# Performance work log

Hardware: AMD Instinct MI355X
Metric: run time of the kernel (lower is better)

The kernel has to match this reference:

```python
import jax, jax.numpy as jnp
import numpy as np

NUM_QUBITS = 10
LAYERS = 8
DIM = 2 ** NUM_QUBITS  # 1024


def _build_entangling(nq: int) -> jnp.ndarray:
    """Static chain-of-CNOTs entangling block, D x D complex64."""
    I = np.eye(2)
    cnot = np.array([[1, 0, 0, 0], [0, 1, 0, 0], [0, 0, 0, 1], [0, 0, 1, 0]], dtype=np.float64)
    M = np.eye(2 ** nq)
    layers = []
    for i in range(nq - 1):
        mats = [I] * nq
        mats[i] = cnot
        del mats[i + 1]
        out = np.eye(1)
        for m in mats:
            out = np.kron(out, m)
        layers.append(out)
    for L in reversed(layers):
        M = L @ M
    return jnp.asarray(M, dtype=jnp.complex64)


ENTANGLING = _build_entangling(NUM_QUBITS)


def _r3(angles):
    # angles: [B, 3] (omega, theta, phi) -> [B, 2, 2] complex64 R3 gate
    omega, theta, phi = angles[:, 0], angles[:, 1], angles[:, 2]
    c = jnp.cos(theta / 2).astype(jnp.complex64)
    s = jnp.sin(theta / 2).astype(jnp.complex64)
    m11 = jnp.exp(-0.5j * (phi + omega)) * c
    m12 = -jnp.exp(0.5j * (phi - omega)) * s
    m21 = jnp.exp(-0.5j * (phi - omega)) * s
    m22 = jnp.exp(0.5j * (phi + omega)) * c
    return jnp.stack([jnp.stack([m11, m12], -1), jnp.stack([m21, m22], -1)], -2)


def _batched_kron(a, b):
    # a: [B, m, n], b: [B, p, q] -> [B, m*p, n*q]
    B = a.shape[0]
    return jnp.einsum('bij,bkl->bikjl', a, b).reshape(B, a.shape[1] * b.shape[1], a.shape[2] * b.shape[2])


def _rotation_block(angles):
    # angles: [copies, num_qubits, 3] -> [copies, D, D] complex64
    out = _r3(angles[:, 0])
    for q in range(1, NUM_QUBITS):
        out = _batched_kron(out, _r3(angles[:, q]))
    return out


def setup_inputs() -> dict:
    key = jax.random.key(0)
    k1, k2 = jax.random.split(key)
    inp = jax.random.normal(k1, (128, DIM), dtype=jnp.float32)
    params = jax.random.normal(k2, (32, LAYERS, NUM_QUBITS, 3), dtype=jnp.float32)
    return {"input": inp, "params": params}


def reference(input, params):
    copies = params.shape[0]
    batch = input.shape[0] // copies
    M0 = jnp.broadcast_to(jnp.eye(DIM, dtype=jnp.complex64), (copies, DIM, DIM))
    xs = jnp.moveaxis(params, 1, 0)  # [layers, copies, nq, 3]

    def step(M, p):
        M = jnp.matmul(_rotation_block(p), M)         # rotation layer
        M = jnp.einsum('ij,bjk->bik', ENTANGLING, M)  # entangling layer
        return M, None

    M, _ = jax.lax.scan(step, M0, xs)
    M = jnp.repeat(M, batch, axis=0)                  # [copies*batch, D, D]
    x = input.astype(jnp.complex64)
    return jnp.einsum('bij,bj->bi', M, x)
```

## Files before the change

kernel.cpp:

```cpp
#include <hip/hip_runtime.h>


#define DIM 1024
#define NQ 10
#define NLAYERS 8
#define NGATES (NLAYERS * NQ)

__device__ __forceinline__ unsigned short f2bf(float f) {
    unsigned int u = __float_as_uint(f);
    unsigned int r = u + 0x7FFFu + ((u >> 16) & 1u);
    return (unsigned short)(r >> 16);
}

__global__ __launch_bounds__(512) void
UnitaryR3Ansatz_18846316495450_kernel(const float* __restrict__ inp,
                                      const float* __restrict__ params,
                                      void* __restrict__ outp,
                                      int out_size)
{
    __shared__ float gates[NGATES][8];
    __shared__ float2 bufA[DIM];
    __shared__ float2 bufB[DIM];

    const int b = blockIdx.x;
    const int c = b >> 2;
    const int t = threadIdx.x;

    if (t < NGATES) {
        const float* p = params + c * (NLAYERS * NQ * 3) + t * 3;
        const float omega = p[0], theta = p[1], phi = p[2];
        float sh, ch;  sincosf(0.5f * theta, &sh, &ch);
        float sa, ca;  sincosf(0.5f * (phi + omega), &sa, &ca);
        float sb, cb;  sincosf(0.5f * (phi - omega), &sb, &cb);
        gates[t][0] = ca * ch;  gates[t][1] = -sa * ch;
        gates[t][2] = -cb * sh; gates[t][3] = -sb * sh;
        gates[t][4] = cb * sh;  gates[t][5] = -sb * sh;
        gates[t][6] = ca * ch;  gates[t][7] = sa * ch;
    }

    const float* x = inp + b * DIM;
    bufA[t]       = make_float2(x[t], 0.0f);
    bufA[t + 512] = make_float2(x[t + 512], 0.0f);

    float2* cur = bufA;
    float2* nxt = bufB;

    for (int l = 0; l < NLAYERS; ++l) {
        for (int q = 0; q < NQ; ++q) {
            __syncthreads();
            const int k = 9 - q;
            const int s = 1 << k;
            const int i0 = ((t >> k) << (k + 1)) | (t & (s - 1));
            const int i1 = i0 | s;
            const float* g = gates[l * NQ + q];
            const float2 a0 = cur[i0];
            const float2 a1 = cur[i1];
            float2 n0, n1;
            n0.x = g[0] * a0.x - g[1] * a0.y + g[2] * a1.x - g[3] * a1.y;
            n0.y = g[0] * a0.y + g[1] * a0.x + g[2] * a1.y + g[3] * a1.x;
            n1.x = g[4] * a0.x - g[5] * a0.y + g[6] * a1.x - g[7] * a1.y;
            n1.y = g[4] * a0.y + g[5] * a0.x + g[6] * a1.y + g[7] * a1.x;
            cur[i0] = n0;
            cur[i1] = n1;
        }
        __syncthreads();
        {
            const int x0 = t, x1 = t + 512;
            nxt[x0 ^ (x0 >> 1)] = cur[x0];
            nxt[x1 ^ (x1 >> 1)] = cur[x1];
        }
        float2* tmp = cur; cur = nxt; nxt = tmp;
    }

    __syncthreads();

    if (out_size >= 2 * DIM * 128) {
        ushort2* o2 = (ushort2*)outp + (size_t)b * DIM;
        for (int j = t; j < DIM; j += 512) {
            ushort2 v; v.x = f2bf(cur[j].x); v.y = f2bf(cur[j].y);
            o2[j] = v;
        }
    } else {
        float* of = (float*)outp + (size_t)b * DIM;
        for (int j = t; j < DIM; j += 512) {
            of[j] = cur[j].x;
        }
    }
}

extern "C" void kernel_launch(void* const* d_in, const int* in_sizes, int n_in,
                              void* d_out, int out_size, void* d_ws, size_t ws_size,
                              hipStream_t stream) {
    const float* inp    = (const float*)d_in[0];
    const float* params = (const float*)d_in[1];
    (void)in_sizes; (void)n_in; (void)d_ws; (void)ws_size;
    UnitaryR3Ansatz_18846316495450_kernel<<<128, 512, 0, stream>>>(inp, params, d_out, out_size);
}
```

Before: 72.12 us.

## Keep state vector in registers of one wavefront, using shuffles for gates

Each block becomes a single 64-lane wavefront that holds 16 amplitudes per lane in registers. Gates on low qubits are applied in-register, gates on high qubits use xor shuffles, and the Gray-code entangling permutation uses shuffles plus register swaps. This removes the 80 block-wide barriers and the shared-memory round-trips per sample. The cost is only 128 wavefronts in total, which leaves the GPU lightly occupied, plus heavy register pressure and many shuffle instructions.

```diff
diff --git a/kernel.cpp b/kernel.cpp
--- a/kernel.cpp
+++ b/kernel.cpp
@@ -4,7 +4,7 @@
 #define DIM 1024
 #define NQ 10
 #define NLAYERS 8
-#define NGATES (NLAYERS * NQ)
+#define NGATES 80
 
 __device__ __forceinline__ unsigned short f2bf(float f) {
     unsigned int u = __float_as_uint(f);
@@ -12,78 +12,135 @@
     return (unsigned short)(r >> 16);
 }
 
-__global__ __launch_bounds__(512) void
+__device__ __forceinline__ float2 cmadd2(float2 c0, float2 x0, float2 c1, float2 x1) {
+    float re = c0.x * x0.x - c0.y * x0.y + c1.x * x1.x - c1.y * x1.y;
+    float im = c0.x * x0.y + c0.y * x0.x + c1.x * x1.y + c1.y * x1.x;
+    return make_float2(re, im);
+}
+
+template <int K>
+__device__ __forceinline__ void local_gate(float2 (&a)[16], float2 m11, float2 m12,
+                                           float2 m21, float2 m22) {
+#pragma unroll
+    for (int p = 0; p < 8; ++p) {
+        const int i0 = ((p >> K) << (K + 1)) | (p & ((1 << K) - 1));
+        const int i1 = i0 | (1 << K);
+        const float2 a0 = a[i0];
+        const float2 a1 = a[i1];
+        a[i0] = cmadd2(m11, a0, m12, a1);
+        a[i1] = cmadd2(m21, a0, m22, a1);
+    }
+}
+
+template <int M>
+__device__ __forceinline__ void cross_gate(float2 (&a)[16], int lane, float2 m11,
+                                           float2 m12, float2 m21, float2 m22) {
+    const bool hi = (lane >> M) & 1;
+    const float2 cs = hi ? m22 : m11;
+    const float2 co = hi ? m21 : m12;
+#pragma unroll
+    for (int r = 0; r < 16; ++r) {
+        float2 o;
+        o.x = __shfl_xor(a[r].x, 1 << M, 64);
+        o.y = __shfl_xor(a[r].y, 1 << M, 64);
+        a[r] = cmadd2(cs, a[r], co, o);
+    }
+}
+
+__device__ __forceinline__ void gray_permute(float2 (&a)[16], int lane) {
+    int S = lane;
+    S ^= S >> 1; S ^= S >> 2; S ^= S >> 4;
+    S &= 63;
+    float2 tmp[16];
+#pragma unroll
+    for (int r = 0; r < 16; ++r) {
+        tmp[r].x = __shfl(a[r].x, S, 64);
+        tmp[r].y = __shfl(a[r].y, S, 64);
+    }
+#pragma unroll
+    for (int t = 0; t < 16; ++t) a[t ^ (t >> 1)] = tmp[t];
+    const bool s0 = S & 1;
+#pragma unroll
+    for (int s = 0; s < 8; ++s) {
+        const float2 lo = a[s], hi2 = a[s + 8];
+        a[s]     = s0 ? hi2 : lo;
+        a[s + 8] = s0 ? lo : hi2;
+    }
+}
+
+__global__ __launch_bounds__(64) void
 UnitaryR3Ansatz_18846316495450_kernel(const float* __restrict__ inp,
                                       const float* __restrict__ params,
                                       void* __restrict__ outp,
                                       int out_size)
 {
-    __shared__ float gates[NGATES][8];
-    __shared__ float2 bufA[DIM];
-    __shared__ float2 bufB[DIM];
+    __shared__ float4 gates[NGATES][2];
 
     const int b = blockIdx.x;
     const int c = b >> 2;
-    const int t = threadIdx.x;
+    const int lane = threadIdx.x;
 
-    if (t < NGATES) {
-        const float* p = params + c * (NLAYERS * NQ * 3) + t * 3;
+    for (int gi = lane; gi < NGATES; gi += 64) {
+        const float* p = params + c * (NGATES * 3) + gi * 3;
         const float omega = p[0], theta = p[1], phi = p[2];
         float sh, ch;  sincosf(0.5f * theta, &sh, &ch);
         float sa, ca;  sincosf(0.5f * (phi + omega), &sa, &ca);
         float sb, cb;  sincosf(0.5f * (phi - omega), &sb, &cb);
-        gates[t][0] = ca * ch;  gates[t][1] = -sa * ch;
-        gates[t][2] = -cb * sh; gates[t][3] = -sb * sh;
-        gates[t][4] = cb * sh;  gates[t][5] = -sb * sh;
-        gates[t][6] = ca * ch;  gates[t][7] = sa * ch;
+        gates[gi][0] = make_float4(ca * ch, -sa * ch, -cb * sh, -sb * sh);
+        gates[gi][1] = make_float4(cb * sh, -sb * sh, ca * ch, sa * ch);
     }
 
-    const float* x = inp + b * DIM;
-    bufA[t]       = make_float2(x[t], 0.0f);
-    bufA[t + 512] = make_float2(x[t + 512], 0.0f);
-
-    float2* cur = bufA;
-    float2* nxt = bufB;
-
-    for (int l = 0; l < NLAYERS; ++l) {
-        for (int q = 0; q < NQ; ++q) {
-            __syncthreads();
-            const int k = 9 - q;
-            const int s = 1 << k;
-            const int i0 = ((t >> k) << (k + 1)) | (t & (s - 1));
-            const int i1 = i0 | s;
-            const float* g = gates[l * NQ + q];
-            const float2 a0 = cur[i0];
-            const float2 a1 = cur[i1];
-            float2 n0, n1;
-            n0.x = g[0] * a0.x - g[1] * a0.y + g[2] * a1.x - g[3] * a1.y;
-            n0.y = g[0] * a0.y + g[1] * a0.x + g[2] * a1.y + g[3] * a1.x;
-            n1.x = g[4] * a0.x - g[5] * a0.y + g[6] * a1.x - g[7] * a1.y;
-            n1.y = g[4] * a0.y + g[5] * a0.x + g[6] * a1.y + g[7] * a1.x;
-            cur[i0] = n0;
-            cur[i1] = n1;
-        }
-        __syncthreads();
-        {
-            const int x0 = t, x1 = t + 512;
-            nxt[x0 ^ (x0 >> 1)] = cur[x0];
-            nxt[x1 ^ (x1 >> 1)] = cur[x1];
-        }
-        float2* tmp = cur; cur = nxt; nxt = tmp;
+    float2 a[16];
+    const float4* xv = (const float4*)(inp + b * DIM + lane * 16);
+#pragma unroll
+    for (int i = 0; i < 4; ++i) {
+        const float4 v = xv[i];
+        a[4 * i + 0] = make_float2(v.x, 0.0f);
+        a[4 * i + 1] = make_float2(v.y, 0.0f);
+        a[4 * i + 2] = make_float2(v.z, 0.0f);
+        a[4 * i + 3] = make_float2(v.w, 0.0f);
     }
 
     __syncthreads();
 
+    for (int l = 0; l < NLAYERS; ++l) {
+        float2 m11, m12, m21, m22;
+#define LOADG(q)                                        \
+        {                                               \
+            const float4 g0 = gates[l * NQ + (q)][0];   \
+            const float4 g1 = gates[l * NQ + (q)][1];   \
+            m11 = make_float2(g0.x, g0.y);              \
+            m12 = make_float2(g0.z, g0.w);              \
+            m21 = make_float2(g1.x, g1.y);              \
+            m22 = make_float2(g1.z, g1.w);              \
+        }
+        LOADG(0); cross_gate<5>(a, lane, m11, m12, m21, m22);
+        LOADG(1); cross_gate<4>(a, lane, m11, m12, m21, m22);
+        LOADG(2); cross_gate<3>(a, lane, m11, m12, m21, m22);
+        LOADG(3); cross_gate<2>(a, lane, m11, m12, m21, m22);
+        LOADG(4); cross_gate<1>(a, lane, m11, m12, m21, m22);
+        LOADG(5); cross_gate<0>(a, lane, m11, m12, m21, m22);
+        LOADG(6); local_gate<3>(a, m11, m12, m21, m22);
+        LOADG(7); local_gate<2>(a, m11, m12, m21, m22);
+        LOADG(8); local_gate<1>(a, m11, m12, m21, m22);
+        LOADG(9); local_gate<0>(a, m11, m12, m21, m22);
+#undef LOADG
+        gray_permute(a, lane);
+    }
+
     if (out_size >= 2 * DIM * 128) {
-        ushort2* o2 = (ushort2*)outp + (size_t)b * DIM;
-        for (int j = t; j < DIM; j += 512) {
-            ushort2 v; v.x = f2bf(cur[j].x); v.y = f2bf(cur[j].y);
-            o2[j] = v;
+        ushort2* o2 = (ushort2*)outp + (size_t)b * DIM + lane * 16;
+#pragma unroll
+        for (int i = 0; i < 16; ++i) {
+            ushort2 v; v.x = f2bf(a[i].x); v.y = f2bf(a[i].y);
+            o2[i] = v;
         }
     } else {
-        float* of = (float*)outp + (size_t)b * DIM;
-        for (int j = t; j < DIM; j += 512) {
-            of[j] = cur[j].x;
+        float4* of = (float4*)((float*)outp + (size_t)b * DIM + lane * 16);
+#pragma unroll
+        for (int i = 0; i < 4; ++i) {
+            of[i] = make_float4(a[4 * i + 0].x, a[4 * i + 1].x,
+                                a[4 * i + 2].x, a[4 * i + 3].x);
         }
     }
 }
@@ -94,5 +151,5 @@
     const float* inp    = (const float*)d_in[0];
     const float* params = (const float*)d_in[1];
     (void)in_sizes; (void)n_in; (void)d_ws; (void)ws_size;
-    UnitaryR3Ansatz_18846316495450_kernel<<<128, 512, 0, stream>>>(inp, params, d_out, out_size);
+    UnitaryR3Ansatz_18846316495450_kernel<<<128, 64, 0, stream>>>(inp, params, d_out, out_size);
 }
```

Measured after the change: 90.03 us. +24.8%, slower.
